# Kernel optimization log

Measured on AMD Instinct MI355X. Metric: run time of the kernel, lower is better.

The kernel has to match this reference:

```python
import jax, jax.numpy as jnp
import numpy as np

EMBED_DIM = 1024


def _lru_init(d, seed=0):
    rng = np.random.default_rng(seed)
    r_min, r_max = 0.9, 0.999
    u1 = rng.random(d)
    u2 = rng.random(d)
    nu_log = np.log(-0.5 * np.log(u1 * (r_max ** 2 - r_min ** 2) + r_min ** 2))
    theta_log = np.log(u2 * np.pi * 2)
    gamma_log = np.log(np.sqrt(1 - np.exp(-np.exp(nu_log)) ** 2))
    return theta_log.astype(np.float32), gamma_log.astype(np.float32)


def setup_inputs() -> dict:
    key = jax.random.key(0)
    ks = jax.random.split(key, 8)
    d = EMBED_DIM
    b, n = 4, 4096
    theta_log, gamma_log = _lru_init(d)
    s = 1.0 / np.sqrt(d)
    s2 = 1.0 / np.sqrt(2 * d)
    return {
        "x": jax.random.normal(ks[0], (b, n, d), dtype=jnp.float32),
        "theta_log": jnp.asarray(theta_log),
        "gamma_log": jnp.asarray(gamma_log),
        "nu_w": jax.random.uniform(ks[1], (d, d), minval=-s, maxval=s, dtype=jnp.float32),
        "nu_b": jax.random.uniform(ks[2], (d,), minval=-s, maxval=s, dtype=jnp.float32),
        "in_w": jax.random.uniform(ks[3], (2 * d, d), minval=-s, maxval=s, dtype=jnp.float32),
        "in_b": jax.random.uniform(ks[4], (2 * d,), minval=-s, maxval=s, dtype=jnp.float32),
        "out_w": jax.random.uniform(ks[5], (d, 2 * d), minval=-s2, maxval=s2, dtype=jnp.float32),
        "out_b": jax.random.uniform(ks[6], (d,), minval=-s2, maxval=s2, dtype=jnp.float32),
    }


def reference(x, theta_log, gamma_log, nu_w, nu_b, in_w, in_b, out_w, out_b):
    # x: (b, n, d) -> (n, b, d)
    xt = jnp.transpose(x, (1, 0, 2))
    n, b, d = xt.shape
    input_state = jnp.einsum("nbd,ed->nbe", xt, in_w) + in_b  # (n, b, 2d)
    nu = jax.nn.sigmoid(jnp.einsum("nbd,ed->nbe", xt, nu_w) + nu_b)  # (n, b, d)
    theta = jnp.exp(theta_log)  # (d,)
    gamma = jnp.exp(gamma_log)  # (d,)
    lam_r = nu * jnp.cos(theta)  # (n, b, d)
    lam_i = nu * jnp.sin(theta)
    # 'n b (e k) -> n b e k' with k=2: even idx = real, odd = imag
    ist = input_state.reshape(n, b, d, 2)
    u_r = gamma * ist[..., 0]
    u_i = gamma * ist[..., 1]

    def step(carry, inp):
        hr, hi = carry
        lr, li, ur, ui = inp
        nhr = lr * hr - li * hi + ur
        nhi = lr * hi + li * hr + ui
        return (nhr, nhi), (nhr, nhi)

    h0 = (jnp.zeros((b, d), x.dtype), jnp.zeros((b, d), x.dtype))
    _, (h_r, h_i) = jax.lax.scan(step, h0, (lam_r, lam_i, u_r, u_i))
    feature = jnp.concatenate([h_r, h_i], axis=-1)  # (n, b, 2d)
    out = jnp.einsum("nbe,de->nbd", feature, out_w) + out_b
    return jnp.transpose(out, (1, 0, 2))  # (b, n, d)
```

## Files before the change

### kernel.cpp

```cpp
#include <hip/hip_runtime.h>
#include <math.h>
#include <stdint.h>

#define BB 4
#define NN 4096
#define DD 1024
#define TT (BB * NN)
#define NC 64
#define CL (NN / NC)

typedef __attribute__((ext_vector_type(8))) short bf16x8;
typedef __attribute__((ext_vector_type(4))) float f32x4;

__device__ inline unsigned short bf_rne(float v) {
  union { float f; uint32_t u; } x; x.f = v;
  uint32_t r = x.u + 0x7fffu + ((x.u >> 16) & 1u);
  return (unsigned short)(r >> 16);
}
__device__ inline float bf_to_f(unsigned short h) {
  union { float f; uint32_t u; } x; x.u = ((uint32_t)h) << 16;
  return x.f;
}

__device__ inline void async16(const void* g, void* l) {
  __builtin_amdgcn_global_load_lds(
      (const __attribute__((address_space(1))) uint32_t*)g,
      (__attribute__((address_space(3))) uint32_t*)l, 16, 0, 0);
}

__global__ __launch_bounds__(256) void conv_x_kernel(
    const float* __restrict__ x, unsigned short* __restrict__ Abf) {
  int idx = blockIdx.x * 256 + threadIdx.x;
  int k = idx & 1023;
  int n = (idx >> 10) & 4095;
  int b = idx >> 22;
  Abf[(size_t)(n * 4 + b) * 1024 + k] = bf_rne(x[idx]);
}

__global__ __launch_bounds__(256) void conv_w1_kernel(
    const float* __restrict__ in_w, const float* __restrict__ nu_w,
    unsigned short* __restrict__ W1) {
  int idx = blockIdx.x * 256 + threadIdx.x;
  float v = (idx < 2048 * 1024) ? in_w[idx] : nu_w[idx - 2048 * 1024];
  W1[idx] = bf_rne(v);
}

__global__ __launch_bounds__(256) void conv_w2_kernel(
    const float* __restrict__ out_w, unsigned short* __restrict__ W2) {
  int idx = blockIdx.x * 256 + threadIdx.x;
  int j = idx >> 10, d = idx & 1023;
  W2[(size_t)j * 2048 + 2 * d]     = bf_rne(out_w[(size_t)j * 2048 + d]);
  W2[(size_t)j * 2048 + 2 * d + 1] = bf_rne(out_w[(size_t)j * 2048 + 1024 + d]);
}

__global__ __launch_bounds__(512, 2) void gemm1_mfma(
    const unsigned short* __restrict__ A,
    const unsigned short* __restrict__ W1,
    const float* __restrict__ in_b, const float* __restrict__ nu_b,
    const float* __restrict__ gamma_log,
    unsigned short* __restrict__ U16, _Float16* __restrict__ NU) {
  __shared__ unsigned short As[2][16384];
  __shared__ unsigned short Bs[2][16384];
  const int tid = threadIdx.x;
  const int w = tid >> 6, l = tid & 63;
  const int q = l >> 4, ml = l & 15;
  const int orig = blockIdx.x + gridDim.x * blockIdx.y;
  const int xcd = orig & 7;
  const int jj_ = orig >> 3;
  const int ntile = jj_ >> 3;
  const int mloc = jj_ & 7;
  const int m0 = (xcd * 8 + mloc) * 256;
  const int n0 = ntile * 256;
  const int wm = w & 1, wn = w >> 1;

  f32x4 acc[8][4] = {};

  auto stage_part = [&](int p, int k0, int c) {
    async16(A  + (size_t)(m0 + c * 64 + l) * 1024 + k0 + w * 8,
            &As[p][(w * 256 + c * 64) * 8]);
    async16(W1 + (size_t)(n0 + c * 64 + l) * 1024 + k0 + w * 8,
            &Bs[p][(w * 256 + c * 64) * 8]);
  };

#pragma unroll
  for (int c = 0; c < 4; ++c) stage_part(0, 0, c);

  int cur = 0;
  for (int k0 = 0; k0 < 1024; k0 += 64) {
    const bool last = (k0 + 64 >= 1024);
    if (!last) {
      stage_part(cur ^ 1, k0 + 64, 0);
      asm volatile("s_waitcnt vmcnt(2)" ::: "memory");
    } else {
      asm volatile("s_waitcnt vmcnt(0)" ::: "memory");
    }
    __builtin_amdgcn_s_barrier();
    __builtin_amdgcn_sched_barrier(0);

    bf16x8 bfr[4], af[4];
#pragma unroll
    for (int ks = 0; ks < 2; ++ks) {
#pragma unroll
      for (int mh = 0; mh < 2; ++mh) {
        if (mh == 0) {
#pragma unroll
          for (int j = 0; j < 4; ++j)
            bfr[j] = *(const bf16x8*)&Bs[cur][(((ks * 4 + q) * 256) + wn * 64 + j * 16 + ml) * 8];
        }
#pragma unroll
        for (int i = 0; i < 4; ++i)
          af[i] = *(const bf16x8*)&As[cur][(((ks * 4 + q) * 256) + wm * 128 + mh * 64 + i * 16 + ml) * 8];
        const int ph = ks * 2 + mh;
        if (!last && ph < 3) stage_part(cur ^ 1, k0 + 64, ph + 1);
        asm volatile("s_waitcnt lgkmcnt(0)" ::: "memory");
        __builtin_amdgcn_sched_barrier(0);
        __builtin_amdgcn_s_setprio(1);
#pragma unroll
        for (int i = 0; i < 4; ++i)
#pragma unroll
          for (int j = 0; j < 4; ++j)
            acc[mh * 4 + i][j] = __builtin_amdgcn_mfma_f32_16x16x32_bf16(
                af[i], bfr[j], acc[mh * 4 + i][j], 0, 0, 0);
        __builtin_amdgcn_s_setprio(0);
        __builtin_amdgcn_sched_barrier(0);
        __builtin_amdgcn_s_barrier();
      }
    }
    cur ^= 1;
  }

  if (n0 < 2048) {
#pragma unroll
    for (int j = 0; j < 4; ++j) {
      int col = n0 + wn * 64 + j * 16 + ml;
      float bias = in_b[col];
      float gam = expf(gamma_log[col >> 1]);
#pragma unroll
      for (int i = 0; i < 8; ++i) {
        int trow = m0 + wm * 128 + i * 16 + q * 4;
#pragma unroll
        for (int v = 0; v < 4; ++v)
          U16[(size_t)(trow + v) * 2048 + col] = bf_rne(gam * (acc[i][j][v] + bias));
      }
    }
  } else {
#pragma unroll
    for (int j = 0; j < 4; ++j) {
      int col = n0 + wn * 64 + j * 16 + ml;
      int c2 = col - 2048;
      float bias = nu_b[c2];
#pragma unroll
      for (int i = 0; i < 8; ++i) {
        int trow = m0 + wm * 128 + i * 16 + q * 4;
#pragma unroll
        for (int v = 0; v < 4; ++v) {
          float z = acc[i][j][v] + bias;
          NU[(size_t)(trow + v) * 1024 + c2] = (_Float16)(1.f / (1.f + expf(-z)));
        }
      }
    }
  }
}

__global__ __launch_bounds__(256) void scan_p1_kernel(
    const unsigned short* __restrict__ U16, const _Float16* __restrict__ NU,
    const float* __restrict__ theta_log,
    float* __restrict__ chunkA) {
  int s = blockIdx.x * 256 + threadIdx.x;
  int dch = s & (DD - 1);
  int b = (s >> 10) & (BB - 1);
  int c = s >> 12;
  float theta = expf(theta_log[dch]);
  float ct = cosf(theta), st = sinf(theta);
  float hr = 0.f, hi = 0.f, Ar = 1.f, Ai = 0.f;
  for (int i = 0; i < CL; ++i) {
    int t = (c * CL + i) * 4 + b;
    ushort2 up = *(const ushort2*)(U16 + (size_t)t * 2048 + 2 * dch);
    float ur = bf_to_f(up.x), ui = bf_to_f(up.y);
    float nu = (float)NU[(size_t)t * 1024 + dch];
    float lr = nu * ct, li = nu * st;
    float hr2 = lr * hr - li * hi + ur;
    float hi2 = lr * hi + li * hr + ui;
    hr = hr2; hi = hi2;
    float Ar2 = lr * Ar - li * Ai;
    float Ai2 = lr * Ai + li * Ar;
    Ar = Ar2; Ai = Ai2;
  }
  float4 o = {Ar, Ai, hr, hi};
  *(float4*)(chunkA + (size_t)s * 4) = o;
}

__global__ __launch_bounds__(256) void scan_p2_kernel(
    float* __restrict__ chunkA) {
  int qx = blockIdx.x * 256 + threadIdx.x;
  int dch = qx & (DD - 1);
  int b = qx >> 10;
  float cr = 0.f, ci = 0.f;
  for (int c = 0; c < NC; ++c) {
    size_t idx = ((size_t)(c * BB + b) * DD + dch) * 4;
    float4 v = *(const float4*)(chunkA + idx);
    float2 wv = {cr, ci};
    *(float2*)(chunkA + idx + 2) = wv;
    float nr = v.x * cr - v.y * ci + v.z;
    float ni = v.x * ci + v.y * cr + v.w;
    cr = nr; ci = ni;
  }
}

__global__ __launch_bounds__(256) void scan_p3_kernel(
    unsigned short* __restrict__ U16, const _Float16* __restrict__ NU,
    const float* __restrict__ theta_log, const float* __restrict__ chunkA) {
  const int c = blockIdx.x >> 2, b = blockIdx.x & 3;
  const int tid = threadIdx.x;
  float ct[4], st[4], hr[4], hi_[4];
#pragma unroll
  for (int dj = 0; dj < 4; ++dj) {
    int d = tid * 4 + dj;
    float th = expf(theta_log[d]);
    ct[dj] = cosf(th); st[dj] = sinf(th);
    const float* cp = chunkA + ((size_t)((c * 4 + b) * 1024) + d) * 4 + 2;
    hr[dj] = cp[0]; hi_[dj] = cp[1];
  }
  for (int i = 0; i < CL; ++i) {
    int t = (c * CL + i) * 4 + b;
    unsigned short* up = U16 + (size_t)t * 2048 + 8 * tid;
    bf16x8 uv = *(const bf16x8*)up;
    const _Float16* nup = NU + (size_t)t * 1024 + 4 * tid;
    bf16x8 fo;
#pragma unroll
    for (int dj = 0; dj < 4; ++dj) {
      float nu = (float)nup[dj];
      float lr = nu * ct[dj], li = nu * st[dj];
      float nhr = lr * hr[dj] - li * hi_[dj] + bf_to_f((unsigned short)uv[2 * dj]);
      float nhi = lr * hi_[dj] + li * hr[dj] + bf_to_f((unsigned short)uv[2 * dj + 1]);
      hr[dj] = nhr; hi_[dj] = nhi;
      fo[2 * dj] = (short)bf_rne(nhr);
      fo[2 * dj + 1] = (short)bf_rne(nhi);
    }
    *(bf16x8*)up = fo;
  }
}

__global__ __launch_bounds__(512, 2) void gemm2_mfma(
    const unsigned short* __restrict__ F,
    const unsigned short* __restrict__ W2,
    const float* __restrict__ out_b,
    float* __restrict__ out) {
  __shared__ unsigned short As[2][16384];
  __shared__ unsigned short Bs[2][16384];
  const int tid = threadIdx.x;
  const int w = tid >> 6, l = tid & 63;
  const int q = l >> 4, ml = l & 15;
  const int orig = blockIdx.x + gridDim.x * blockIdx.y;
  const int xcd = orig & 7;
  const int jj_ = orig >> 3;
  const int mloc = jj_ >> 2;
  const int ntile = jj_ & 3;
  const int m0 = (xcd * 8 + mloc) * 256;
  const int n0 = ntile * 256;
  const int wm = w & 1, wn = w >> 1;

  f32x4 acc[8][4] = {};

  auto stage_part = [&](int p, int k0, int c) {
    async16(F  + (size_t)(m0 + c * 64 + l) * 2048 + k0 + w * 8,
            &As[p][(w * 256 + c * 64) * 8]);
    async16(W2 + (size_t)(n0 + c * 64 + l) * 2048 + k0 + w * 8,
            &Bs[p][(w * 256 + c * 64) * 8]);
  };

#pragma unroll
  for (int c = 0; c < 4; ++c) stage_part(0, 0, c);

  int cur = 0;
  for (int k0 = 0; k0 < 2048; k0 += 64) {
    const bool last = (k0 + 64 >= 2048);
    if (!last) {
      stage_part(cur ^ 1, k0 + 64, 0);
      asm volatile("s_waitcnt vmcnt(2)" ::: "memory");
    } else {
      asm volatile("s_waitcnt vmcnt(0)" ::: "memory");
    }
    __builtin_amdgcn_s_barrier();
    __builtin_amdgcn_sched_barrier(0);

    bf16x8 bfr[4], af[4];
#pragma unroll
    for (int ks = 0; ks < 2; ++ks) {
#pragma unroll
      for (int mh = 0; mh < 2; ++mh) {
        if (mh == 0) {
#pragma unroll
          for (int j = 0; j < 4; ++j)
            bfr[j] = *(const bf16x8*)&Bs[cur][(((ks * 4 + q) * 256) + wn * 64 + j * 16 + ml) * 8];
        }
#pragma unroll
        for (int i = 0; i < 4; ++i)
          af[i] = *(const bf16x8*)&As[cur][(((ks * 4 + q) * 256) + wm * 128 + mh * 64 + i * 16 + ml) * 8];
        const int ph = ks * 2 + mh;
        if (!last && ph < 3) stage_part(cur ^ 1, k0 + 64, ph + 1);
        asm volatile("s_waitcnt lgkmcnt(0)" ::: "memory");
        __builtin_amdgcn_sched_barrier(0);
        __builtin_amdgcn_s_setprio(1);
#pragma unroll
        for (int i = 0; i < 4; ++i)
#pragma unroll
          for (int j = 0; j < 4; ++j)
            acc[mh * 4 + i][j] = __builtin_amdgcn_mfma_f32_16x16x32_bf16(
                af[i], bfr[j], acc[mh * 4 + i][j], 0, 0, 0);
        __builtin_amdgcn_s_setprio(0);
        __builtin_amdgcn_sched_barrier(0);
        __builtin_amdgcn_s_barrier();
      }
    }
    cur ^= 1;
  }

#pragma unroll
  for (int j = 0; j < 4; ++j) {
    int col = n0 + wn * 64 + j * 16 + ml;
    float bias = out_b[col];
#pragma unroll
    for (int i = 0; i < 8; ++i) {
      int trow = m0 + wm * 128 + i * 16 + q * 4;
#pragma unroll
      for (int v = 0; v < 4; ++v) {
        int t = trow + v;
        out[((size_t)(t & 3) * NN + (t >> 2)) * DD + col] = acc[i][j][v] + bias;
      }
    }
  }
}

extern "C" void kernel_launch(void* const* d_in, const int* in_sizes, int n_in,
                              void* d_out, int out_size, void* d_ws, size_t ws_size,
                              hipStream_t stream) {
  const float* x         = (const float*)d_in[0];
  const float* theta_log = (const float*)d_in[1];
  const float* gamma_log = (const float*)d_in[2];
  const float* nu_w      = (const float*)d_in[3];
  const float* nu_b      = (const float*)d_in[4];
  const float* in_w      = (const float*)d_in[5];
  const float* in_b      = (const float*)d_in[6];
  const float* out_w     = (const float*)d_in[7];
  const float* out_b     = (const float*)d_in[8];
  float* out = (float*)d_out;

  char* base = (char*)d_ws;
  unsigned short* U16 = (unsigned short*)base;
  _Float16*       NU  = (_Float16*)(base + 67108864);
  unsigned short* Abf = (unsigned short*)(base + 100663296);
  unsigned short* W1  = (unsigned short*)(base + 134217728);
  unsigned short* W2  = (unsigned short*)(base + 140509184);
  float*          chunkA = (float*)(base + 144703488);

  conv_x_kernel<<<(BB * NN * DD) / 256, 256, 0, stream>>>(x, Abf);
  conv_w1_kernel<<<(3072 * 1024) / 256, 256, 0, stream>>>(in_w, nu_w, W1);
  conv_w2_kernel<<<(1024 * 1024) / 256, 256, 0, stream>>>(out_w, W2);
  gemm1_mfma<<<dim3(3072 / 256, TT / 256), 512, 0, stream>>>(
      Abf, W1, in_b, nu_b, gamma_log, U16, NU);
  scan_p1_kernel<<<(NC * BB * DD) / 256, 256, 0, stream>>>(U16, NU, theta_log, chunkA);
  scan_p2_kernel<<<(BB * DD) / 256, 256, 0, stream>>>(chunkA);
  scan_p3_kernel<<<NC * BB, 256, 0, stream>>>(U16, NU, theta_log, chunkA);
  gemm2_mfma<<<dim3(1024 / 256, TT / 256), 512, 0, stream>>>(U16, W2, out_b, out);
}
```

Before: 490.9 us.

## Vectorize x conversion, merge weight conversions, and widen scan phase-3 grid

The x-to-bf16 conversion now processes four floats per thread with vector loads and stores. The two weight conversion kernels are merged into one launch. Scan phase 3 now gives each thread a single channel across four times as many blocks, where before each thread handled four channels in 256 blocks. This raises occupancy for the sequential inner loop, at the cost of narrower per-thread memory accesses.

New measurement: 466.6 us. 5.0% less time.

```diff
diff --git a/kernel.cpp b/kernel.cpp
--- a/kernel.cpp
+++ b/kernel.cpp
@@ -31,26 +31,28 @@
 __global__ __launch_bounds__(256) void conv_x_kernel(
     const float* __restrict__ x, unsigned short* __restrict__ Abf) {
   int idx = blockIdx.x * 256 + threadIdx.x;
-  int k = idx & 1023;
-  int n = (idx >> 10) & 4095;
-  int b = idx >> 22;
-  Abf[(size_t)(n * 4 + b) * 1024 + k] = bf_rne(x[idx]);
-}
-
-__global__ __launch_bounds__(256) void conv_w1_kernel(
+  int k4 = idx & 255;
+  int n = (idx >> 8) & 4095;
+  int b = idx >> 20;
+  float4 v = ((const float4*)x)[idx];
+  ushort4 o = {bf_rne(v.x), bf_rne(v.y), bf_rne(v.z), bf_rne(v.w)};
+  *(ushort4*)(Abf + (size_t)(n * 4 + b) * 1024 + k4 * 4) = o;
+}
+
+__global__ __launch_bounds__(256) void conv_w_kernel(
     const float* __restrict__ in_w, const float* __restrict__ nu_w,
-    unsigned short* __restrict__ W1) {
+    const float* __restrict__ out_w,
+    unsigned short* __restrict__ W1, unsigned short* __restrict__ W2) {
   int idx = blockIdx.x * 256 + threadIdx.x;
-  float v = (idx < 2048 * 1024) ? in_w[idx] : nu_w[idx - 2048 * 1024];
-  W1[idx] = bf_rne(v);
-}
-
-__global__ __launch_bounds__(256) void conv_w2_kernel(
-    const float* __restrict__ out_w, unsigned short* __restrict__ W2) {
-  int idx = blockIdx.x * 256 + threadIdx.x;
-  int j = idx >> 10, d = idx & 1023;
-  W2[(size_t)j * 2048 + 2 * d]     = bf_rne(out_w[(size_t)j * 2048 + d]);
-  W2[(size_t)j * 2048 + 2 * d + 1] = bf_rne(out_w[(size_t)j * 2048 + 1024 + d]);
+  if (idx < 3072 * 1024) {
+    float v = (idx < 2048 * 1024) ? in_w[idx] : nu_w[idx - 2048 * 1024];
+    W1[idx] = bf_rne(v);
+  } else {
+    int t = idx - 3072 * 1024;
+    int j = t >> 10, d = t & 1023;
+    W2[(size_t)j * 2048 + 2 * d]     = bf_rne(out_w[(size_t)j * 2048 + d]);
+    W2[(size_t)j * 2048 + 2 * d + 1] = bf_rne(out_w[(size_t)j * 2048 + 1024 + d]);
+  }
 }
 
 __global__ __launch_bounds__(512, 2) void gemm1_mfma(
@@ -210,34 +212,24 @@
 __global__ __launch_bounds__(256) void scan_p3_kernel(
     unsigned short* __restrict__ U16, const _Float16* __restrict__ NU,
     const float* __restrict__ theta_log, const float* __restrict__ chunkA) {
-  const int c = blockIdx.x >> 2, b = blockIdx.x & 3;
-  const int tid = threadIdx.x;
-  float ct[4], st[4], hr[4], hi_[4];
-#pragma unroll
-  for (int dj = 0; dj < 4; ++dj) {
-    int d = tid * 4 + dj;
-    float th = expf(theta_log[d]);
-    ct[dj] = cosf(th); st[dj] = sinf(th);
-    const float* cp = chunkA + ((size_t)((c * 4 + b) * 1024) + d) * 4 + 2;
-    hr[dj] = cp[0]; hi_[dj] = cp[1];
-  }
+  const int quarter = blockIdx.x & 3;
+  const int b = (blockIdx.x >> 2) & 3;
+  const int c = blockIdx.x >> 4;
+  const int d = quarter * 256 + threadIdx.x;
+  float th = expf(theta_log[d]);
+  float ct = cosf(th), st = sinf(th);
+  const float* cp = chunkA + ((size_t)((c * 4 + b) * 1024) + d) * 4 + 2;
+  float hr = cp[0], hi = cp[1];
   for (int i = 0; i < CL; ++i) {
     int t = (c * CL + i) * 4 + b;
-    unsigned short* up = U16 + (size_t)t * 2048 + 8 * tid;
-    bf16x8 uv = *(const bf16x8*)up;
-    const _Float16* nup = NU + (size_t)t * 1024 + 4 * tid;
-    bf16x8 fo;
-#pragma unroll
-    for (int dj = 0; dj < 4; ++dj) {
-      float nu = (float)nup[dj];
-      float lr = nu * ct[dj], li = nu * st[dj];
-      float nhr = lr * hr[dj] - li * hi_[dj] + bf_to_f((unsigned short)uv[2 * dj]);
-      float nhi = lr * hi_[dj] + li * hr[dj] + bf_to_f((unsigned short)uv[2 * dj + 1]);
-      hr[dj] = nhr; hi_[dj] = nhi;
-      fo[2 * dj] = (short)bf_rne(nhr);
-      fo[2 * dj + 1] = (short)bf_rne(nhi);
-    }
-    *(bf16x8*)up = fo;
+    ushort2 uv = *(const ushort2*)(U16 + (size_t)t * 2048 + 2 * d);
+    float nu = (float)NU[(size_t)t * 1024 + d];
+    float lr = nu * ct, li = nu * st;
+    float nhr = lr * hr - li * hi + bf_to_f(uv.x);
+    float nhi = lr * hi + li * hr + bf_to_f(uv.y);
+    hr = nhr; hi = nhi;
+    ushort2 o = {bf_rne(nhr), bf_rne(nhi)};
+    *(ushort2*)(U16 + (size_t)t * 2048 + 2 * d) = o;
   }
 }
 
@@ -354,13 +346,13 @@
   unsigned short* W2  = (unsigned short*)(base + 140509184);
   float*          chunkA = (float*)(base + 144703488);
 
-  conv_x_kernel<<<(BB * NN * DD) / 256, 256, 0, stream>>>(x, Abf);
-  conv_w1_kernel<<<(3072 * 1024) / 256, 256, 0, stream>>>(in_w, nu_w, W1);
-  conv_w2_kernel<<<(1024 * 1024) / 256, 256, 0, stream>>>(out_w, W2);
+  conv_x_kernel<<<(BB * NN * DD / 4) / 256, 256, 0, stream>>>(x, Abf);
+  conv_w_kernel<<<(3072 * 1024 + 1024 * 1024) / 256, 256, 0, stream>>>(
+      in_w, nu_w, out_w, W1, W2);
   gemm1_mfma<<<dim3(3072 / 256, TT / 256), 512, 0, stream>>>(
       Abf, W1, in_b, nu_b, gamma_log, U16, NU);
   scan_p1_kernel<<<(NC * BB * DD) / 256, 256, 0, stream>>>(U16, NU, theta_log, chunkA);
   scan_p2_kernel<<<(BB * DD) / 256, 256, 0, stream>>>(chunkA);
-  scan_p3_kernel<<<NC * BB, 256, 0, stream>>>(U16, NU, theta_log, chunkA);
+  scan_p3_kernel<<<NC * BB * 4, 256, 0, stream>>>(U16, NU, theta_log, chunkA);
   gemm2_mfma<<<dim3(1024 / 256, TT / 256), 512, 0, stream>>>(U16, W2, out_b, out);
 }
```
